# Optimization experiments

Hardware: AMD Instinct MI355X
Metric: run time of the kernel (lower is better)

Reference implementation:

```python
import jax, jax.numpy as jnp
import numpy as np

B, IN, D = 4096, 2048, 2048
NAMES = ["inpgate", "rec_inpgate", "mem_inpgate", "inp", "rec_inp", "readgate",
         "rec_readgate", "mem_readgate", "decoder", "writegate", "rec_writegate",
         "mem_writegate", "encoder"]


def setup_inputs() -> dict:
    key = jax.random.key(0)
    ks = jax.random.split(key, 1 + len(NAMES))
    inp = {
        "x": jax.random.normal(ks[0], (B, IN), jnp.float32),
        "out0": jnp.zeros((B, D), jnp.float32),   # recurrent output state (reset())
        "mem0": jnp.zeros((B, D), jnp.float32),   # memory state (reset())
    }
    for i, n in enumerate(NAMES):
        inp["w_" + n] = jax.random.normal(ks[1 + i], (D, D), jnp.float32) * 0.02
        inp["b_" + n] = jnp.zeros((D,), jnp.float32)
    return inp


def _lin(v, W, b):
    # torch nn.Linear: y = v @ W.T + b, W is [out, in]
    return v @ W.T + b


def reference(x, out0, mem0,
              w_inpgate, b_inpgate, w_rec_inpgate, b_rec_inpgate,
              w_mem_inpgate, b_mem_inpgate, w_inp, b_inp,
              w_rec_inp, b_rec_inp, w_readgate, b_readgate,
              w_rec_readgate, b_rec_readgate, w_mem_readgate, b_mem_readgate,
              w_decoder, b_decoder, w_writegate, b_writegate,
              w_rec_writegate, b_rec_writegate, w_mem_writegate, b_mem_writegate,
              w_encoder, b_encoder):
    sig = jax.nn.sigmoid
    # input block (note: original uses sigmoid here, not tanh)
    block_inp = sig(_lin(x, w_inp, b_inp) + _lin(out0, w_rec_inp, b_rec_inp))
    inp_gate = sig(_lin(x, w_inpgate, b_inpgate)
                   + _lin(mem0, w_mem_inpgate, b_mem_inpgate)
                   + _lin(out0, w_rec_inpgate, b_rec_inpgate))
    read_gate = sig(_lin(x, w_readgate, b_readgate)
                    + _lin(mem0, w_mem_readgate, b_mem_readgate)
                    + _lin(out0, w_rec_readgate, b_rec_readgate))
    decoded_mem = _lin(read_gate * mem0, w_decoder, b_decoder)
    hidden = decoded_mem + block_inp * inp_gate
    write_gate = sig(_lin(x, w_writegate, b_writegate)
                     + _lin(mem0, w_mem_writegate, b_mem_writegate)
                     + _lin(out0, w_rec_writegate, b_rec_writegate))
    enc = jnp.tanh(_lin(hidden, w_encoder, b_encoder))
    mem = (1.0 - write_gate) * mem0 + write_gate * enc
    # torch forward() returns self.out (== hidden_act); mem is internal state
    return hidden
```

## Files before the change

### kernel.cpp

```cpp
#include <hip/hip_runtime.h>
#include <stdint.h>


typedef short bf16x8 __attribute__((ext_vector_type(8)));
typedef float f32x4 __attribute__((ext_vector_type(4)));

#define AS1(p) ((__attribute__((address_space(1))) void*)(uintptr_t)(p))
#define AS3(p) ((__attribute__((address_space(3))) void*)(uint32_t)(uintptr_t)(p))
#define GLD16(gp, lp) __builtin_amdgcn_global_load_lds(AS1(gp), AS3(lp), 16, 0, 0)

__device__ __forceinline__ unsigned short f2bf(float f) {
  union { float f; unsigned u; } c; c.f = f;
  unsigned u = c.u;
  unsigned r = (u + 0x7FFFu + ((u >> 16) & 1u)) >> 16;
  return (unsigned short)r;
}
__device__ __forceinline__ float bf2f(unsigned short h) {
  union { unsigned u; float f; } c; c.u = ((unsigned)h) << 16;
  return c.f;
}
__device__ __forceinline__ float sigf(float x) {
  return 1.0f / (1.0f + __expf(-x));
}

__global__ void init_flags_kernel(int* flags) {
  if (threadIdx.x < 2) flags[threadIdx.x] = 0;
}

struct ConvActArgs {
  const float4* src[3];
  ushort4* dst[3];
  int flagidx[3];
  int n4;
  int* flags;
};

__global__ void conv_acts_kernel(ConvActArgs a) {
  const int arr = blockIdx.y;
  const float4* __restrict__ s = a.src[arr];
  ushort4* __restrict__ d = a.dst[arr];
  unsigned nz = 0;
  for (int i = blockIdx.x * blockDim.x + threadIdx.x; i < a.n4;
       i += gridDim.x * blockDim.x) {
    float4 v = s[i];
    union { float f; unsigned u; } cx, cy, cz, cw;
    cx.f = v.x; cy.f = v.y; cz.f = v.z; cw.f = v.w;
    nz |= cx.u | cy.u | cz.u | cw.u;
    ushort4 o;
    o.x = f2bf(v.x); o.y = f2bf(v.y); o.z = f2bf(v.z); o.w = f2bf(v.w);
    d[i] = o;
  }
  const int fi = a.flagidx[arr];
  if (fi >= 0) {
    if (__any(nz != 0u) && (threadIdx.x & 63) == 0) atomicOr(&a.flags[fi], 1);
  }
}

struct ConvWArgs {
  const float4* src[9];
  ushort4* dst[9];
  int flagidx[9];
  int n4;
  const int* flags;
};

__global__ void conv_weights_kernel(ConvWArgs a) {
  const int arr = blockIdx.y;
  const int fi = a.flagidx[arr];
  if (fi >= 0 && a.flags[fi] == 0) return;
  const float4* __restrict__ s = a.src[arr];
  ushort4* __restrict__ d = a.dst[arr];
  for (int i = blockIdx.x * blockDim.x + threadIdx.x; i < a.n4;
       i += gridDim.x * blockDim.x) {
    float4 v = s[i];
    ushort4 o;
    o.x = f2bf(v.x); o.y = f2bf(v.y); o.z = f2bf(v.z); o.w = f2bf(v.w);
    d[i] = o;
  }
}

struct DualArgs {
  const unsigned short *xb, *o0b, *m0b;
  const unsigned short *Winp, *Wrecinp, *Winpgate, *Wrecinpgate, *Wmeminpgate;
  const float *b_inp, *b_rec_inp, *b_inpgate, *b_rec_inpgate, *b_mem_inpgate;
  const float* b_dec;
  const int* flags;
  unsigned short *u1, *u2;
  float* outF;
};

__global__ void __launch_bounds__(256, 2)
gemm_dual(DualArgs a) {
  __shared__ __attribute__((aligned(16))) unsigned short sA[128 * 64];
  __shared__ __attribute__((aligned(16))) unsigned short sB1[128 * 64];
  __shared__ __attribute__((aligned(16))) unsigned short sB2[128 * 64];

  const int tid = threadIdx.x;
  const int l = tid & 63;
  const int w = tid >> 6;
  const int wm = w >> 1, wn = w & 1;
  const int bm = blockIdx.y, bn = blockIdx.x;

  f32x4 acc1[4][4], acc2[4][4];
#pragma unroll
  for (int i = 0; i < 4; ++i)
#pragma unroll
    for (int j = 0; j < 4; ++j) {
      acc1[i][j] = (f32x4){0.f, 0.f, 0.f, 0.f};
      acc2[i][j] = (f32x4){0.f, 0.f, 0.f, 0.f};
    }

  const int srow = l >> 3;
  const int kchS = (l & 7) ^ srow;
  const long long laneA = ((long long)bm * 128 + srow) * 2048 + kchS * 8;
  const long long laneB = ((long long)bn * 128 + srow) * 2048 + kchS * 8;

  auto do_dual = [&](const unsigned short* Ap, const unsigned short* W1p,
                     const unsigned short* W2p) {
    const unsigned short* ga = Ap + laneA;
    const unsigned short* g1 = W1p + laneB;
    const unsigned short* g2 = W2p + laneB;
    for (int kt = 0; kt < 32; ++kt) {
#pragma unroll
      for (int ii = 0; ii < 4; ++ii) {
        const int q = w * 4 + ii;
        GLD16(ga + (long long)(q * 8) * 2048, (char*)sA + q * 1024);
        GLD16(g1 + (long long)(q * 8) * 2048, (char*)sB1 + q * 1024);
        GLD16(g2 + (long long)(q * 8) * 2048, (char*)sB2 + q * 1024);
      }
      __syncthreads();
#pragma unroll
      for (int ks = 0; ks < 2; ++ks) {
        bf16x8 af[4], b1[4], b2[4];
        const int c = ks * 4 + (l >> 4);
#pragma unroll
        for (int i = 0; i < 4; ++i) {
          const int ra = wm * 64 + i * 16 + (l & 15);
          const int rb = wn * 64 + i * 16 + (l & 15);
          af[i] = *(const bf16x8*)((const char*)sA + (ra * 128 + ((c ^ (ra & 7)) * 16)));
          b1[i] = *(const bf16x8*)((const char*)sB1 + (rb * 128 + ((c ^ (rb & 7)) * 16)));
          b2[i] = *(const bf16x8*)((const char*)sB2 + (rb * 128 + ((c ^ (rb & 7)) * 16)));
        }
#pragma unroll
        for (int i = 0; i < 4; ++i)
#pragma unroll
          for (int j = 0; j < 4; ++j) {
            acc1[i][j] = __builtin_amdgcn_mfma_f32_16x16x32_bf16(
                af[i], b1[j], acc1[i][j], 0, 0, 0);
            acc2[i][j] = __builtin_amdgcn_mfma_f32_16x16x32_bf16(
                af[i], b2[j], acc2[i][j], 0, 0, 0);
          }
      }
      __syncthreads();
      ga += 64; g1 += 64; g2 += 64;
    }
  };

  auto do_single2 = [&](const unsigned short* Ap, const unsigned short* Wp) {
    const unsigned short* ga = Ap + laneA;
    const unsigned short* gb = Wp + laneB;
    for (int kt = 0; kt < 32; ++kt) {
#pragma unroll
      for (int ii = 0; ii < 4; ++ii) {
        const int q = w * 4 + ii;
        GLD16(ga + (long long)(q * 8) * 2048, (char*)sA + q * 1024);
        GLD16(gb + (long long)(q * 8) * 2048, (char*)sB2 + q * 1024);
      }
      __syncthreads();
#pragma unroll
      for (int ks = 0; ks < 2; ++ks) {
        bf16x8 af[4], b2[4];
        const int c = ks * 4 + (l >> 4);
#pragma unroll
        for (int i = 0; i < 4; ++i) {
          const int ra = wm * 64 + i * 16 + (l & 15);
          const int rb = wn * 64 + i * 16 + (l & 15);
          af[i] = *(const bf16x8*)((const char*)sA + (ra * 128 + ((c ^ (ra & 7)) * 16)));
          b2[i] = *(const bf16x8*)((const char*)sB2 + (rb * 128 + ((c ^ (rb & 7)) * 16)));
        }
#pragma unroll
        for (int i = 0; i < 4; ++i)
#pragma unroll
          for (int j = 0; j < 4; ++j)
            acc2[i][j] = __builtin_amdgcn_mfma_f32_16x16x32_bf16(
                af[i], b2[j], acc2[i][j], 0, 0, 0);
      }
      __syncthreads();
      ga += 64; gb += 64;
    }
  };

  const int f_out0 = a.flags[0];
  const int f_mem0 = a.flags[1];

  do_dual(a.xb, a.Winp, a.Winpgate);
  if (f_out0) do_dual(a.o0b, a.Wrecinp, a.Wrecinpgate);
  if (f_mem0) do_single2(a.m0b, a.Wmeminpgate);

  const int colb = bn * 128 + wn * 64;
  const int rowb = bm * 128 + wm * 64;
  const bool fast = (f_mem0 == 0);
#pragma unroll
  for (int j = 0; j < 4; ++j) {
    const int col = colb + j * 16 + (l & 15);
    const float s1 = a.b_inp[col] + a.b_rec_inp[col];
    const float s2 = a.b_inpgate[col] + a.b_rec_inpgate[col] + a.b_mem_inpgate[col];
    const float bd = fast ? a.b_dec[col] : 0.f;
#pragma unroll
    for (int i = 0; i < 4; ++i) {
      const int row0 = rowb + i * 16 + (l >> 4) * 4;
#pragma unroll
      for (int r = 0; r < 4; ++r) {
        const long long idx = (long long)(row0 + r) * 2048 + col;
        const float u1v = acc1[i][j][r] + s1;
        const float u2v = acc2[i][j][r] + s2;
        if (fast) {
          a.outF[idx] = sigf(u1v) * sigf(u2v) + bd;
        } else {
          a.u1[idx] = f2bf(u1v);
          a.u2[idx] = f2bf(u2v);
        }
      }
    }
  }
}

struct Job {
  const unsigned short* A0; const unsigned short* W0; const float* b0;
  const unsigned short* A1; const unsigned short* W1; const float* b1;
  const unsigned short* A2; const unsigned short* W2; const float* b2;
  int f0, f1, f2;
  int npairs;
  int jobf;
  const int* flags;
  const float* add;
  float* outF;
  unsigned short* outH;
};

__global__ void __launch_bounds__(256)
gemm_bt_multi(Job jb) {
  __shared__ __attribute__((aligned(16))) unsigned short sA[128 * 64];
  __shared__ __attribute__((aligned(16))) unsigned short sB[128 * 64];

  if (jb.jobf >= 0 && jb.flags[jb.jobf] == 0) return;

  const int tid = threadIdx.x;
  const int l = tid & 63;
  const int w = tid >> 6;
  const int wm = w >> 1, wn = w & 1;
  const int bm = blockIdx.y, bn = blockIdx.x;

  f32x4 acc[4][4];
#pragma unroll
  for (int i = 0; i < 4; ++i)
#pragma unroll
    for (int j = 0; j < 4; ++j) acc[i][j] = (f32x4){0.f, 0.f, 0.f, 0.f};

  const int srow = l >> 3;
  const int kchS = (l & 7) ^ srow;
  const long long laneA = ((long long)bm * 128 + srow) * 2048 + kchS * 8;
  const long long laneB = ((long long)bn * 128 + srow) * 2048 + kchS * 8;

  auto do_pair = [&](const unsigned short* Ap, const unsigned short* Wp) {
    const unsigned short* ga = Ap + laneA;
    const unsigned short* gb = Wp + laneB;
    for (int kt = 0; kt < 32; ++kt) {
#pragma unroll
      for (int ii = 0; ii < 4; ++ii) {
        const int q = w * 4 + ii;
        GLD16(ga + (long long)(q * 8) * 2048, (char*)sA + q * 1024);
        GLD16(gb + (long long)(q * 8) * 2048, (char*)sB + q * 1024);
      }
      __syncthreads();
#pragma unroll
      for (int ks = 0; ks < 2; ++ks) {
        bf16x8 af[4], bf[4];
        const int c = ks * 4 + (l >> 4);
#pragma unroll
        for (int i = 0; i < 4; ++i) {
          const int ra = wm * 64 + i * 16 + (l & 15);
          const int rb = wn * 64 + i * 16 + (l & 15);
          af[i] = *(const bf16x8*)((const char*)sA + (ra * 128 + ((c ^ (ra & 7)) * 16)));
          bf[i] = *(const bf16x8*)((const char*)sB + (rb * 128 + ((c ^ (rb & 7)) * 16)));
        }
#pragma unroll
        for (int i = 0; i < 4; ++i)
#pragma unroll
          for (int j = 0; j < 4; ++j)
            acc[i][j] = __builtin_amdgcn_mfma_f32_16x16x32_bf16(
                af[i], bf[j], acc[i][j], 0, 0, 0);
      }
      __syncthreads();
      ga += 64;
      gb += 64;
    }
  };

  if (jb.f0 < 0 || jb.flags[jb.f0]) do_pair(jb.A0, jb.W0);
  if (jb.npairs > 1 && (jb.f1 < 0 || jb.flags[jb.f1])) do_pair(jb.A1, jb.W1);
  if (jb.npairs > 2 && (jb.f2 < 0 || jb.flags[jb.f2])) do_pair(jb.A2, jb.W2);

  const int colb = bn * 128 + wn * 64;
  const int rowb = bm * 128 + wm * 64;
#pragma unroll
  for (int j = 0; j < 4; ++j) {
    const int col = colb + j * 16 + (l & 15);
    float bias = 0.f;
    if (jb.b0) bias += jb.b0[col];
    if (jb.npairs > 1 && jb.b1) bias += jb.b1[col];
    if (jb.npairs > 2 && jb.b2) bias += jb.b2[col];
#pragma unroll
    for (int i = 0; i < 4; ++i) {
      const int row0 = rowb + i * 16 + (l >> 4) * 4;
#pragma unroll
      for (int r = 0; r < 4; ++r) {
        const long long idx = (long long)(row0 + r) * 2048 + col;
        float v = acc[i][j][r] + bias;
        if (jb.add) v += jb.add[idx];
        if (jb.outF) jb.outF[idx] = v;
        else jb.outH[idx] = f2bf(v);
      }
    }
  }
}

__global__ void gates_kernel(const ushort4* __restrict__ u1,
                             const ushort4* __restrict__ u2,
                             const ushort4* __restrict__ u3,
                             const float4* __restrict__ mem0,
                             float4* __restrict__ g, ushort4* __restrict__ rg,
                             const int* flags, int n4) {
  if (flags[1] == 0) return;
  int i = blockIdx.x * blockDim.x + threadIdx.x;
  if (i >= n4) return;
  ushort4 a = u1[i], b = u2[i], c = u3[i];
  float4 m = mem0[i];
  float4 go;
  ushort4 ro;
  go.x = sigf(bf2f(a.x)) * sigf(bf2f(b.x)); ro.x = f2bf(sigf(bf2f(c.x)) * m.x);
  go.y = sigf(bf2f(a.y)) * sigf(bf2f(b.y)); ro.y = f2bf(sigf(bf2f(c.y)) * m.y);
  go.z = sigf(bf2f(a.z)) * sigf(bf2f(b.z)); ro.z = f2bf(sigf(bf2f(c.z)) * m.z);
  go.w = sigf(bf2f(a.w)) * sigf(bf2f(b.w)); ro.w = f2bf(sigf(bf2f(c.w)) * m.w);
  g[i] = go;
  rg[i] = ro;
}

extern "C" void kernel_launch(void* const* d_in, const int* in_sizes, int n_in,
                              void* d_out, int out_size, void* d_ws, size_t ws_size,
                              hipStream_t stream) {
  (void)in_sizes; (void)n_in; (void)out_size; (void)ws_size;
  const int Bx = 4096, Dx = 2048;
  const size_t ACT = (size_t)Bx * Dx;
  const size_t WEL = (size_t)Dx * Dx;

  const float* x    = (const float*)d_in[0];
  const float* out0 = (const float*)d_in[1];
  const float* mem0 = (const float*)d_in[2];
  const float* w_inpgate     = (const float*)d_in[3];
  const float* b_inpgate     = (const float*)d_in[4];
  const float* w_rec_inpgate = (const float*)d_in[5];
  const float* b_rec_inpgate = (const float*)d_in[6];
  const float* w_mem_inpgate = (const float*)d_in[7];
  const float* b_mem_inpgate = (const float*)d_in[8];
  const float* w_inp         = (const float*)d_in[9];
  const float* b_inp         = (const float*)d_in[10];
  const float* w_rec_inp     = (const float*)d_in[11];
  const float* b_rec_inp     = (const float*)d_in[12];
  const float* w_readgate    = (const float*)d_in[13];
  const float* b_readgate    = (const float*)d_in[14];
  const float* w_rec_readgate= (const float*)d_in[15];
  const float* b_rec_readgate= (const float*)d_in[16];
  const float* w_mem_readgate= (const float*)d_in[17];
  const float* b_mem_readgate= (const float*)d_in[18];
  const float* w_decoder     = (const float*)d_in[19];
  const float* b_decoder     = (const float*)d_in[20];

  char* ws = (char*)d_ws;
  unsigned short* xb  = (unsigned short*)(ws);
  unsigned short* o0b = xb + ACT;
  unsigned short* m0b = o0b + ACT;
  unsigned short* wb  = m0b + ACT;
  unsigned short* u1 = wb + 9 * WEL;
  unsigned short* u2 = u1 + ACT;
  unsigned short* u3 = u2 + ACT;
  float* g = (float*)(u3 + ACT);
  unsigned short* rg = (unsigned short*)(g + ACT);
  int* flags = (int*)(rg + ACT);

  init_flags_kernel<<<1, 64, 0, stream>>>(flags);

  ConvActArgs aa;
  aa.src[0] = (const float4*)x;    aa.dst[0] = (ushort4*)xb;  aa.flagidx[0] = -1;
  aa.src[1] = (const float4*)out0; aa.dst[1] = (ushort4*)o0b; aa.flagidx[1] = 0;
  aa.src[2] = (const float4*)mem0; aa.dst[2] = (ushort4*)m0b; aa.flagidx[2] = 1;
  aa.n4 = (int)(ACT / 4);
  aa.flags = flags;
  conv_acts_kernel<<<dim3(2048, 3, 1), 256, 0, stream>>>(aa);

  ConvWArgs wa;
  const float* wsrc[9] = {w_inp, w_rec_inp, w_inpgate, w_mem_inpgate,
                          w_rec_inpgate, w_readgate, w_mem_readgate,
                          w_rec_readgate, w_decoder};
  const int wflag[9] = {-1, 0, -1, 1, 0, 1, 1, 0, 1};
  for (int i = 0; i < 9; ++i) {
    wa.src[i] = (const float4*)wsrc[i];
    wa.dst[i] = (ushort4*)(wb + (size_t)i * WEL);
    wa.flagidx[i] = wflag[i];
  }
  wa.n4 = (int)(WEL / 4);
  wa.flags = flags;
  conv_weights_kernel<<<dim3(1024, 9, 1), 256, 0, stream>>>(wa);

  DualArgs da;
  da.xb = xb; da.o0b = o0b; da.m0b = m0b;
  da.Winp = wb + 0 * WEL;      da.Wrecinp = wb + 1 * WEL;
  da.Winpgate = wb + 2 * WEL;  da.Wrecinpgate = wb + 4 * WEL;
  da.Wmeminpgate = wb + 3 * WEL;
  da.b_inp = b_inp; da.b_rec_inp = b_rec_inp;
  da.b_inpgate = b_inpgate; da.b_rec_inpgate = b_rec_inpgate;
  da.b_mem_inpgate = b_mem_inpgate;
  da.b_dec = b_decoder;
  da.flags = flags;
  da.u1 = u1; da.u2 = u2;
  da.outF = (float*)d_out;
  gemm_dual<<<dim3(16, 32, 1), 256, 0, stream>>>(da);

  Job J2 = {};
  J2.A0 = xb;  J2.W0 = wb + 5 * WEL; J2.b0 = b_readgate;      J2.f0 = -1;
  J2.A1 = m0b; J2.W1 = wb + 6 * WEL; J2.b1 = b_mem_readgate;  J2.f1 = 1;
  J2.A2 = o0b; J2.W2 = wb + 7 * WEL; J2.b2 = b_rec_readgate;  J2.f2 = 0;
  J2.npairs = 3; J2.jobf = 1; J2.flags = flags; J2.outH = u3;
  gemm_bt_multi<<<dim3(16, 32, 1), 256, 0, stream>>>(J2);

  gates_kernel<<<(int)(ACT / 4 + 255) / 256, 256, 0, stream>>>(
      (const ushort4*)u1, (const ushort4*)u2, (const ushort4*)u3,
      (const float4*)mem0, (float4*)g, (ushort4*)rg, flags, (int)(ACT / 4));

  Job JD = {};
  JD.A0 = rg; JD.W0 = wb + 8 * WEL; JD.b0 = b_decoder; JD.f0 = 1;
  JD.npairs = 1; JD.jobf = 1; JD.flags = flags;
  JD.add = g; JD.outF = (float*)d_out;
  gemm_bt_multi<<<dim3(16, 32, 1), 256, 0, stream>>>(JD);
}
```

Measured before the change: 366.9 us.

## Double-buffer dual GEMM with 256x128 tiles, 8 waves and interleaved prefetch

Rewrites the gemm_dual kernel to use 512 threads with 256x128 output tiles and double-buffered LDS. The next K-tile's global-to-LDS loads are spread across the four MFMA phases of the current tile, with explicit waitcnt, barriers and setprio used to overlap memory and compute. The larger tile raises reuse of the weight tiles, and the grid is halved. LDS use rises to about 128KB per block, which likely limits occupancy to one block per CU despite the launch bound of two.

```diff
diff --git a/kernel.cpp b/kernel.cpp
--- a/kernel.cpp
+++ b/kernel.cpp
@@ -8,6 +8,8 @@
 #define AS1(p) ((__attribute__((address_space(1))) void*)(uintptr_t)(p))
 #define AS3(p) ((__attribute__((address_space(3))) void*)(uint32_t)(uintptr_t)(p))
 #define GLD16(gp, lp) __builtin_amdgcn_global_load_lds(AS1(gp), AS3(lp), 16, 0, 0)
+
+template <bool B> struct BoolC { static constexpr bool value = B; };
 
 __device__ __forceinline__ unsigned short f2bf(float f) {
   union { float f; unsigned u; } c; c.f = f;
@@ -89,131 +91,196 @@
   float* outF;
 };
 
-__global__ void __launch_bounds__(256, 2)
+__global__ void __launch_bounds__(512, 2)
 gemm_dual(DualArgs a) {
-  __shared__ __attribute__((aligned(16))) unsigned short sA[128 * 64];
-  __shared__ __attribute__((aligned(16))) unsigned short sB1[128 * 64];
-  __shared__ __attribute__((aligned(16))) unsigned short sB2[128 * 64];
+  __shared__ __attribute__((aligned(16))) unsigned short sA[2][256 * 64];
+  __shared__ __attribute__((aligned(16))) unsigned short sB1[2][128 * 64];
+  __shared__ __attribute__((aligned(16))) unsigned short sB2[2][128 * 64];
 
   const int tid = threadIdx.x;
   const int l = tid & 63;
   const int w = tid >> 6;
-  const int wm = w >> 1, wn = w & 1;
+  const int wm = w >> 2, wn = w & 3;
   const int bm = blockIdx.y, bn = blockIdx.x;
 
-  f32x4 acc1[4][4], acc2[4][4];
-#pragma unroll
-  for (int i = 0; i < 4; ++i)
-#pragma unroll
-    for (int j = 0; j < 4; ++j) {
+  f32x4 acc1[8][2], acc2[8][2];
+#pragma unroll
+  for (int i = 0; i < 8; ++i)
+#pragma unroll
+    for (int j = 0; j < 2; ++j) {
       acc1[i][j] = (f32x4){0.f, 0.f, 0.f, 0.f};
       acc2[i][j] = (f32x4){0.f, 0.f, 0.f, 0.f};
     }
 
   const int srow = l >> 3;
   const int kchS = (l & 7) ^ srow;
-  const long long laneA = ((long long)bm * 128 + srow) * 2048 + kchS * 8;
-  const long long laneB = ((long long)bn * 128 + srow) * 2048 + kchS * 8;
-
-  auto do_dual = [&](const unsigned short* Ap, const unsigned short* W1p,
-                     const unsigned short* W2p) {
+  const long long laneA = ((long long)(bm * 256) + srow) * 2048 + kchS * 8;
+  const long long laneB = ((long long)(bn * 128) + srow) * 2048 + kchS * 8;
+
+  const int rB = w * 16;
+  const int rA0 = (w & 3) * 16 + (w >> 2) * 128;
+
+  auto run_pass = [&](auto dc, const unsigned short* Ap,
+                      const unsigned short* W1p, const unsigned short* W2p) {
+    constexpr bool DUAL = decltype(dc)::value;
     const unsigned short* ga = Ap + laneA;
-    const unsigned short* g1 = W1p + laneB;
+    const unsigned short* g1 = DUAL ? (W1p + laneB) : (const unsigned short*)0;
     const unsigned short* g2 = W2p + laneB;
-    for (int kt = 0; kt < 32; ++kt) {
-#pragma unroll
-      for (int ii = 0; ii < 4; ++ii) {
-        const int q = w * 4 + ii;
-        GLD16(ga + (long long)(q * 8) * 2048, (char*)sA + q * 1024);
-        GLD16(g1 + (long long)(q * 8) * 2048, (char*)sB1 + q * 1024);
-        GLD16(g2 + (long long)(q * 8) * 2048, (char*)sB2 + q * 1024);
+
+    if constexpr (DUAL) {
+      GLD16(g1 + (long long)rB * 2048,       (char*)sB1[0] + rB * 128);
+      GLD16(g1 + (long long)(rB + 8) * 2048, (char*)sB1[0] + (rB + 8) * 128);
+    }
+    GLD16(g2 + (long long)rB * 2048,         (char*)sB2[0] + rB * 128);
+    GLD16(g2 + (long long)(rB + 8) * 2048,   (char*)sB2[0] + (rB + 8) * 128);
+    GLD16(ga + (long long)rA0 * 2048,        (char*)sA[0] + rA0 * 128);
+    GLD16(ga + (long long)(rA0 + 8) * 2048,  (char*)sA[0] + (rA0 + 8) * 128);
+    GLD16(ga + (long long)(rA0 + 64) * 2048, (char*)sA[0] + (rA0 + 64) * 128);
+    GLD16(ga + (long long)(rA0 + 72) * 2048, (char*)sA[0] + (rA0 + 72) * 128);
+    asm volatile("s_waitcnt vmcnt(2)" ::: "memory");
+    __builtin_amdgcn_s_barrier();
+
+    for (int kt = 0; kt < 31; ++kt) {
+      const int cur = kt & 1, nxt = cur ^ 1;
+      const unsigned short* gan = ga + 64;
+      const unsigned short* g1n = g1 + (DUAL ? 64 : 0);
+      const unsigned short* g2n = g2 + 64;
+#pragma unroll
+      for (int p = 0; p < 4; ++p) {
+        const int ks = p >> 1, ih = p & 1;
+        bf16x8 af[4], b1f[2], b2f[2];
+        const int c = ks * 4 + (l >> 4);
+#pragma unroll
+        for (int i = 0; i < 4; ++i) {
+          const int ra = wm * 128 + ih * 64 + i * 16 + (l & 15);
+          af[i] = *(const bf16x8*)((const char*)sA[cur] +
+                                   (ra * 128 + ((c ^ (ra & 7)) * 16)));
+        }
+#pragma unroll
+        for (int j = 0; j < 2; ++j) {
+          const int rb = wn * 32 + j * 16 + (l & 15);
+          if constexpr (DUAL)
+            b1f[j] = *(const bf16x8*)((const char*)sB1[cur] +
+                                      (rb * 128 + ((c ^ (rb & 7)) * 16)));
+          b2f[j] = *(const bf16x8*)((const char*)sB2[cur] +
+                                    (rb * 128 + ((c ^ (rb & 7)) * 16)));
+        }
+        if constexpr (DUAL) {
+          if (p == 0) {
+            GLD16(g1n + (long long)rB * 2048,       (char*)sB1[nxt] + rB * 128);
+            GLD16(g1n + (long long)(rB + 8) * 2048, (char*)sB1[nxt] + (rB + 8) * 128);
+          } else if (p == 1) {
+            GLD16(g2n + (long long)rB * 2048,       (char*)sB2[nxt] + rB * 128);
+            GLD16(g2n + (long long)(rB + 8) * 2048, (char*)sB2[nxt] + (rB + 8) * 128);
+          } else if (p == 2) {
+            GLD16(gan + (long long)rA0 * 2048,       (char*)sA[nxt] + rA0 * 128);
+            GLD16(gan + (long long)(rA0 + 8) * 2048, (char*)sA[nxt] + (rA0 + 8) * 128);
+          } else {
+            GLD16(gan + (long long)(rA0 + 64) * 2048, (char*)sA[nxt] + (rA0 + 64) * 128);
+            GLD16(gan + (long long)(rA0 + 72) * 2048, (char*)sA[nxt] + (rA0 + 72) * 128);
+          }
+        } else {
+          if (p == 0) {
+            GLD16(g2n + (long long)rB * 2048,       (char*)sB2[nxt] + rB * 128);
+            GLD16(g2n + (long long)(rB + 8) * 2048, (char*)sB2[nxt] + (rB + 8) * 128);
+          } else if (p == 1) {
+            GLD16(gan + (long long)rA0 * 2048,       (char*)sA[nxt] + rA0 * 128);
+            GLD16(gan + (long long)(rA0 + 8) * 2048, (char*)sA[nxt] + (rA0 + 8) * 128);
+          } else if (p == 2) {
+            GLD16(gan + (long long)(rA0 + 64) * 2048, (char*)sA[nxt] + (rA0 + 64) * 128);
+            GLD16(gan + (long long)(rA0 + 72) * 2048, (char*)sA[nxt] + (rA0 + 72) * 128);
+          }
+        }
+        __builtin_amdgcn_s_barrier();
+        asm volatile("s_waitcnt lgkmcnt(0)" ::: "memory");
+        __builtin_amdgcn_s_setprio(1);
+#pragma unroll
+        for (int i = 0; i < 4; ++i)
+#pragma unroll
+          for (int j = 0; j < 2; ++j) {
+            if constexpr (DUAL)
+              acc1[ih * 4 + i][j] = __builtin_amdgcn_mfma_f32_16x16x32_bf16(
+                  af[i], b1f[j], acc1[ih * 4 + i][j], 0, 0, 0);
+            acc2[ih * 4 + i][j] = __builtin_amdgcn_mfma_f32_16x16x32_bf16(
+                af[i], b2f[j], acc2[ih * 4 + i][j], 0, 0, 0);
+          }
+        __builtin_amdgcn_s_setprio(0);
+        if (p == 0 || p == 3)
+          asm volatile("s_waitcnt vmcnt(2)" ::: "memory");
+        __builtin_amdgcn_s_barrier();
       }
-      __syncthreads();
-#pragma unroll
-      for (int ks = 0; ks < 2; ++ks) {
-        bf16x8 af[4], b1[4], b2[4];
+      ga += 64;
+      if constexpr (DUAL) g1 += 64;
+      g2 += 64;
+    }
+
+    {
+      const int cur = 1;
+#pragma unroll
+      for (int p = 0; p < 4; ++p) {
+        const int ks = p >> 1, ih = p & 1;
+        bf16x8 af[4], b1f[2], b2f[2];
         const int c = ks * 4 + (l >> 4);
 #pragma unroll
         for (int i = 0; i < 4; ++i) {
-          const int ra = wm * 64 + i * 16 + (l & 15);
-          const int rb = wn * 64 + i * 16 + (l & 15);
-          af[i] = *(const bf16x8*)((const char*)sA + (ra * 128 + ((c ^ (ra & 7)) * 16)));
-          b1[i] = *(const bf16x8*)((const char*)sB1 + (rb * 128 + ((c ^ (rb & 7)) * 16)));
-          b2[i] = *(const bf16x8*)((const char*)sB2 + (rb * 128 + ((c ^ (rb & 7)) * 16)));
-        }
+          const int ra = wm * 128 + ih * 64 + i * 16 + (l & 15);
+          af[i] = *(const bf16x8*)((const char*)sA[cur] +
+                                   (ra * 128 + ((c ^ (ra & 7)) * 16)));
+        }
+#pragma unroll
+        for (int j = 0; j < 2; ++j) {
+          const int rb = wn * 32 + j * 16 + (l & 15);
+          if constexpr (DUAL)
+            b1f[j] = *(const bf16x8*)((const char*)sB1[cur] +
+                                      (rb * 128 + ((c ^ (rb & 7)) * 16)));
+          b2f[j] = *(const bf16x8*)((const char*)sB2[cur] +
+                                    (rb * 128 + ((c ^ (rb & 7)) * 16)));
+        }
+        __builtin_amdgcn_s_barrier();
+        asm volatile("s_waitcnt lgkmcnt(0)" ::: "memory");
+        __builtin_amdgcn_s_setprio(1);
 #pragma unroll
         for (int i = 0; i < 4; ++i)
 #pragma unroll
-          for (int j = 0; j < 4; ++j) {
-            acc1[i][j] = __builtin_amdgcn_mfma_f32_16x16x32_bf16(
-                af[i], b1[j], acc1[i][j], 0, 0, 0);
-            acc2[i][j] = __builtin_amdgcn_mfma_f32_16x16x32_bf16(
-                af[i], b2[j], acc2[i][j], 0, 0, 0);
+          for (int j = 0; j < 2; ++j) {
+            if constexpr (DUAL)
+              acc1[ih * 4 + i][j] = __builtin_amdgcn_mfma_f32_16x16x32_bf16(
+                  af[i], b1f[j], acc1[ih * 4 + i][j], 0, 0, 0);
+            acc2[ih * 4 + i][j] = __builtin_amdgcn_mfma_f32_16x16x32_bf16(
+                af[i], b2f[j], acc2[ih * 4 + i][j], 0, 0, 0);
           }
+        __builtin_amdgcn_s_setprio(0);
+        if (p == 0)
+          asm volatile("s_waitcnt vmcnt(0)" ::: "memory");
+        __builtin_amdgcn_s_barrier();
       }
-      __syncthreads();
-      ga += 64; g1 += 64; g2 += 64;
-    }
-  };
-
-  auto do_single2 = [&](const unsigned short* Ap, const unsigned short* Wp) {
-    const unsigned short* ga = Ap + laneA;
-    const unsigned short* gb = Wp + laneB;
-    for (int kt = 0; kt < 32; ++kt) {
-#pragma unroll
-      for (int ii = 0; ii < 4; ++ii) {
-        const int q = w * 4 + ii;
-        GLD16(ga + (long long)(q * 8) * 2048, (char*)sA + q * 1024);
-        GLD16(gb + (long long)(q * 8) * 2048, (char*)sB2 + q * 1024);
-      }
-      __syncthreads();
-#pragma unroll
-      for (int ks = 0; ks < 2; ++ks) {
-        bf16x8 af[4], b2[4];
-        const int c = ks * 4 + (l >> 4);
-#pragma unroll
-        for (int i = 0; i < 4; ++i) {
-          const int ra = wm * 64 + i * 16 + (l & 15);
-          const int rb = wn * 64 + i * 16 + (l & 15);
-          af[i] = *(const bf16x8*)((const char*)sA + (ra * 128 + ((c ^ (ra & 7)) * 16)));
-          b2[i] = *(const bf16x8*)((const char*)sB2 + (rb * 128 + ((c ^ (rb & 7)) * 16)));
-        }
-#pragma unroll
-        for (int i = 0; i < 4; ++i)
-#pragma unroll
-          for (int j = 0; j < 4; ++j)
-            acc2[i][j] = __builtin_amdgcn_mfma_f32_16x16x32_bf16(
-                af[i], b2[j], acc2[i][j], 0, 0, 0);
-      }
-      __syncthreads();
-      ga += 64; gb += 64;
     }
   };
 
   const int f_out0 = a.flags[0];
   const int f_mem0 = a.flags[1];
 
-  do_dual(a.xb, a.Winp, a.Winpgate);
-  if (f_out0) do_dual(a.o0b, a.Wrecinp, a.Wrecinpgate);
-  if (f_mem0) do_single2(a.m0b, a.Wmeminpgate);
-
-  const int colb = bn * 128 + wn * 64;
-  const int rowb = bm * 128 + wm * 64;
+  run_pass(BoolC<true>{}, a.xb, a.Winp, a.Winpgate);
+  if (f_out0) run_pass(BoolC<true>{}, a.o0b, a.Wrecinp, a.Wrecinpgate);
+  if (f_mem0) run_pass(BoolC<false>{}, a.m0b, (const unsigned short*)0, a.Wmeminpgate);
+
+  const int colb = bn * 128 + wn * 32;
+  const int rowb = bm * 256 + wm * 128;
   const bool fast = (f_mem0 == 0);
 #pragma unroll
-  for (int j = 0; j < 4; ++j) {
+  for (int j = 0; j < 2; ++j) {
     const int col = colb + j * 16 + (l & 15);
     const float s1 = a.b_inp[col] + a.b_rec_inp[col];
     const float s2 = a.b_inpgate[col] + a.b_rec_inpgate[col] + a.b_mem_inpgate[col];
     const float bd = fast ? a.b_dec[col] : 0.f;
 #pragma unroll
-    for (int i = 0; i < 4; ++i) {
-      const int row0 = rowb + i * 16 + (l >> 4) * 4;
+    for (int ii = 0; ii < 8; ++ii) {
+      const int row0 = rowb + (ii >> 2) * 64 + (ii & 3) * 16 + (l >> 4) * 4;
 #pragma unroll
       for (int r = 0; r < 4; ++r) {
         const long long idx = (long long)(row0 + r) * 2048 + col;
-        const float u1v = acc1[i][j][r] + s1;
-        const float u2v = acc2[i][j][r] + s2;
+        const float u1v = acc1[ii][j][r] + s1;
+        const float u2v = acc2[ii][j][r] + s2;
         if (fast) {
           a.outF[idx] = sigf(u1v) * sigf(u2v) + bd;
         } else {
@@ -424,7 +491,7 @@
   da.flags = flags;
   da.u1 = u1; da.u2 = u2;
   da.outF = (float*)d_out;
-  gemm_dual<<<dim3(16, 32, 1), 256, 0, stream>>>(da);
+  gemm_dual<<<dim3(16, 16, 1), 512, 0, stream>>>(da);
 
   Job J2 = {};
   J2.A0 = xb;  J2.W0 = wb + 5 * WEL; J2.b0 = b_readgate;      J2.f0 = -1;
```

New measurement: 370.3 us. No clear change (+0.9%).
